# Kernel optimization log

Hardware: AMD Instinct MI355X
Metric: run time of the kernel (lower is better)

The kernel has to match this reference:

```python
import jax, jax.numpy as jnp
import numpy as np

NUM_EMB = 512
EMB_DIM = 64
BETA = 0.25


def _conv(x, w, b, stride, pad):
    # x: NCHW, w: OIHW
    y = jax.lax.conv_general_dilated(
        x, w, window_strides=(stride, stride),
        padding=[(pad, pad), (pad, pad)],
        dimension_numbers=('NCHW', 'OIHW', 'NCHW'))
    return y + b[None, :, None, None]


def _deconv(x, w, b, stride, pad, k):
    # torch ConvTranspose2d weight is [in, out, kh, kw]; flip spatially,
    # swap to OIHW, and run a fractionally-strided (lhs-dilated) conv.
    wt = jnp.flip(w, axis=(2, 3)).transpose(1, 0, 2, 3)
    p = k - 1 - pad
    y = jax.lax.conv_general_dilated(
        x, wt, window_strides=(1, 1),
        padding=[(p, p), (p, p)],
        lhs_dilation=(stride, stride),
        dimension_numbers=('NCHW', 'OIHW', 'NCHW'))
    return y + b[None, :, None, None]


def setup_inputs() -> dict:
    key = jax.random.key(0)
    ks = jax.random.split(key, 16)
    s = 0.05
    inp = {
        'x': jax.random.normal(ks[0], (32, 3, 256, 256), jnp.float32),
        # encoder
        'w1': jax.random.normal(ks[1], (64, 3, 4, 4), jnp.float32) * s,
        'b1': jnp.zeros((64,), jnp.float32),
        'w2': jax.random.normal(ks[2], (128, 64, 4, 4), jnp.float32) * s,
        'b2': jnp.zeros((128,), jnp.float32),
        'w3': jax.random.normal(ks[3], (EMB_DIM, 128, 3, 3), jnp.float32) * s,
        'b3': jnp.zeros((EMB_DIM,), jnp.float32),
        # codebook, uniform(-1/N, 1/N) as in torch init
        'emb': jax.random.uniform(ks[4], (NUM_EMB, EMB_DIM), jnp.float32,
                                  -1.0 / NUM_EMB, 1.0 / NUM_EMB),
        # decoder (ConvTranspose2d weights: [in, out, kh, kw])
        'dw1': jax.random.normal(ks[5], (EMB_DIM, 128, 4, 4), jnp.float32) * s,
        'db1': jnp.zeros((128,), jnp.float32),
        'dw2': jax.random.normal(ks[6], (128, 64, 4, 4), jnp.float32) * s,
        'db2': jnp.zeros((64,), jnp.float32),
        'dw3': jax.random.normal(ks[7], (64, 3, 3, 3), jnp.float32) * s,
        'db3': jnp.zeros((3,), jnp.float32),
    }
    return inp


def _forward(x, w1, b1, w2, b2, w3, b3, emb, dw1, db1, dw2, db2, dw3, db3):
    # encoder
    h = jax.nn.relu(_conv(x, w1, b1, 2, 1))
    h = jax.nn.relu(_conv(h, w2, b2, 2, 1))
    z = jax.nn.relu(_conv(h, w3, b3, 1, 1))      # [B, D, H/4, W/4]
    z = z.transpose(0, 2, 3, 1)                   # NHWC
    # vector quantize
    flat = z.reshape(-1, EMB_DIM)                 # [N, D]
    d = (jnp.sum(flat * flat, axis=1, keepdims=True)
         - 2.0 * flat @ emb.T
         + jnp.sum(emb * emb, axis=1))            # [N, K]
    idx = jnp.argmin(d, axis=1)
    q = emb[idx].reshape(z.shape)
    sg = jax.lax.stop_gradient
    loss = jnp.mean((sg(q) - z) ** 2) + BETA * jnp.mean((q - sg(z)) ** 2)
    q = z + sg(q - z)                             # straight-through
    q = q.transpose(0, 3, 1, 2)                   # NCHW
    # decoder
    h = jax.nn.relu(_deconv(q, dw1, db1, 2, 1, 4))
    h = jax.nn.relu(_deconv(h, dw2, db2, 2, 1, 4))
    x_recon = jax.nn.sigmoid(_deconv(h, dw3, db3, 1, 1, 3))
    return x_recon, loss


def reference(x, w1, b1, w2, b2, w3, b3, emb, dw1, db1, dw2, db2, dw3, db3):
    return _forward(x, w1, b1, w2, b2, w3, b3, emb,
                    dw1, db1, dw2, db2, dw3, db3)
```

## Files before the change

### kernel.cpp

```cpp
#include <hip/hip_runtime.h>
#include <math.h>


typedef __attribute__((ext_vector_type(8))) short bf16x8;
typedef __attribute__((ext_vector_type(4))) float fx4;
typedef unsigned short ushort_t;
#define MFMA16(a, b, c) __builtin_amdgcn_mfma_f32_16x16x32_bf16(a, b, c, 0, 0, 0)

__device__ inline ushort_t f2bf(float f) {
    unsigned u = __float_as_uint(f);
    u += 0x7FFFu + ((u >> 16) & 1u);
    return (ushort_t)(u >> 16);
}
__device__ inline float bf2f(ushort_t h) {
    return __uint_as_float(((unsigned)h) << 16);
}

__device__ __forceinline__ void stage16(const ushort_t* g, ushort_t* l) {
#if __has_builtin(__builtin_amdgcn_global_load_lds)
    __builtin_amdgcn_global_load_lds(
        (const __attribute__((address_space(1))) unsigned int*)g,
        (__attribute__((address_space(3))) unsigned int*)l, 16, 0, 0);
#else
    int lane = threadIdx.x & 63;
    *(int4*)(l + lane * 8) = *(const int4*)g;
#endif
}

__device__ __forceinline__ int swz(int s) { return s ^ ((s >> 3) & 7); }
__device__ __forceinline__ bf16x8 sld(const ushort_t* sm, int gslot) {
    return *(const bf16x8*)(sm + (size_t)swz(gslot) * 8);
}

__device__ __forceinline__ void halo_do(
    ushort_t* __restrict__ buf, int B, int H, int W, int C8, int idx)
{
    int perim = 2 * W + 2 * (H - 2);
    int c8 = idx % C8;
    int t = idx / C8;
    int p = t % perim;
    int b = t / perim;
    int r, col;
    if (p < W) { r = 0; col = p; }
    else if (p < 2 * W) { r = H - 1; col = p - W; }
    else { int pp = p - 2 * W; r = 1 + (pp >> 1); col = (pp & 1) ? (W - 1) : 0; }
    size_t off = ((((size_t)b * H + r) * W + col) * C8 + c8) * 8;
    *(int4*)(buf + off) = (int4){0, 0, 0, 0};
}

__global__ __launch_bounds__(256) void halo3_k(
    ushort_t* __restrict__ xp, ushort_t* __restrict__ h2p, ushort_t* __restrict__ qpad)
{
    int i = blockIdx.x * 256 + threadIdx.x;
    if (i < 132096) halo_do(xp, 32, 130, 130, 8, i);
    else if (i < 265216) halo_do(h2p, 32, 66, 66, 16, i - 132096);
    else if (i < 331776) halo_do(qpad, 32, 66, 66, 8, i - 265216);
}
__global__ __launch_bounds__(256) void halo2_k(
    ushort_t* __restrict__ d1c, ushort_t* __restrict__ d2c)
{
    int i = blockIdx.x * 256 + threadIdx.x;
    if (i < 132096) halo_do(d1c, 16, 130, 130, 16, i);
    else if (i < 263680) halo_do(d2c, 16, 258, 258, 8, i - 132096);
}

__global__ __launch_bounds__(256) void cast_x4(
    const float* __restrict__ x, ushort_t* __restrict__ x4)
{
    if (blockIdx.x < 8192) {
        int i = blockIdx.x * 256 + threadIdx.x;
        int w = i & 255, h = (i >> 8) & 255, b = i >> 16;
        size_t base = ((size_t)b * 3 * 256 + h) * 256 + w;
        float v0 = x[base];
        float v1 = x[base + 65536];
        float v2 = x[base + 131072];
        uint2 o;
        o.x = (unsigned)f2bf(v0) | ((unsigned)f2bf(v1) << 16);
        o.y = (unsigned)f2bf(v2);
        *(uint2*)(x4 + ((size_t)(b * 258 + h + 1) * 258 + (w + 1)) * 4) = o;
    } else {
        int idx = (blockIdx.x - 8192) * 256 + threadIdx.x;
        if (idx >= 32 * 1032) return;
        int b = idx / 1032;
        int s = idx % 1032;
        int side = s / 258, c = s % 258;
        int r, col;
        if (side == 0) { r = 0; col = c; }
        else if (side == 1) { r = 257; col = c; }
        else if (side == 2) { r = c; col = 0; }
        else { r = c; col = 257; }
        *(uint2*)(x4 + ((size_t)(b * 258 + r) * 258 + col) * 4) = (uint2){0, 0};
    }
}

__global__ __launch_bounds__(256) void repack_all(
    const float* __restrict__ w1, const float* __restrict__ w2,
    const float* __restrict__ w3, const float* __restrict__ dw1,
    const float* __restrict__ dw2, const float* __restrict__ dw3,
    const float* __restrict__ emb,
    ushort_t* __restrict__ o1, ushort_t* __restrict__ o2,
    ushort_t* __restrict__ o3, ushort_t* __restrict__ od1,
    ushort_t* __restrict__ od2, ushort_t* __restrict__ od3,
    ushort_t* __restrict__ embb, float* __restrict__ se2,
    float* __restrict__ lac)
{
    int gi = blockIdx.x * 256 + threadIdx.x;
    if (gi < 4096) {
        int i = gi;
        int j = i & 7, lane = (i >> 3) & 63, tc = i >> 9;
        int c = tc & 1, t = tc >> 1;
        int co = t * 16 + (lane & 15);
        int k = c * 32 + (lane >> 4) * 8 + j;
        int kh = k >> 4, kw = (k >> 2) & 3, ci = k & 3;
        o1[i] = (ci < 3) ? f2bf(w1[((co * 3 + ci) * 4 + kh) * 4 + kw]) : (ushort_t)0;
    } else if (gi < 135168) {
        int i = gi - 4096;
        int j = i & 7, lane = (i >> 3) & 63, tc = i >> 9;
        int c = tc & 31, t = tc >> 5;
        int co = t * 16 + (lane & 15);
        int k = c * 32 + (lane >> 4) * 8 + j;
        int tap = k >> 6, ci = k & 63, kh = tap >> 2, kw = tap & 3;
        o2[i] = f2bf(w2[((co * 64 + ci) * 4 + kh) * 4 + kw]);
    } else if (gi < 208896) {
        int i = gi - 135168;
        int j = i & 7, lane = (i >> 3) & 63, tc = i >> 9;
        int c = tc % 36, t = tc / 36;
        int co = t * 16 + (lane & 15);
        int k = c * 32 + (lane >> 4) * 8 + j;
        int tap = k >> 7, ci = k & 127, kh = tap / 3, kw = tap % 3;
        o3[i] = f2bf(w3[((co * 128 + ci) * 3 + kh) * 3 + kw]);
    } else if (gi < 339968) {
        int i = gi - 208896;
        int j = i & 7, lane = (i >> 3) & 63, tc = i >> 9;
        int c = tc & 31, t = tc >> 5;
        int co = t * 16 + (lane & 15);
        int k = c * 32 + (lane >> 4) * 8 + j;
        int tap = k >> 6, ci = k & 63, kh = tap >> 2, kw = tap & 3;
        od1[i] = f2bf(dw1[((ci * 128 + co) * 4 + kh) * 4 + kw]);
    } else if (gi < 471040) {
        int i = gi - 339968;
        int j = i & 7, lane = (i >> 3) & 63, tc = i >> 9;
        int c = tc & 63, t = tc >> 6;
        int co = t * 16 + (lane & 15);
        int k = c * 32 + (lane >> 4) * 8 + j;
        int tap = k >> 7, ci = k & 127, kh = tap >> 2, kw = tap & 3;
        od2[i] = f2bf(dw2[((ci * 64 + co) * 4 + kh) * 4 + kw]);
    } else if (gi < 480256) {
        int i = gi - 471040;
        int j = i & 7, lane = (i >> 3) & 63, c = i >> 9;
        int co = lane & 15;
        int k = c * 32 + (lane >> 4) * 8 + j;
        int tap = k >> 6, ci = k & 63, kh = tap / 3, kw = tap % 3;
        od3[i] = (co < 3) ? f2bf(dw3[((ci * 3 + co) * 3 + kh) * 3 + kw]) : (ushort_t)0;
    } else if (gi < 513024) {
        int i = gi - 480256;
        int j = i & 7, lane = (i >> 3) & 63, c = (i >> 9) & 1, nt = i >> 10;
        int n = nt * 16 + (lane & 15);
        int k = c * 32 + (lane >> 4) * 8 + j;
        embb[i] = f2bf(emb[n * 64 + k]);
    } else if (gi < 513536) {
        int n = gi - 513024;
        const float* e = emb + n * 64;
        float s = 0.f;
        for (int d = 0; d < 64; ++d) s = fmaf(e[d], e[d], s);
        se2[n] = s;
    } else if (gi == 513536) {
        lac[0] = 0.f;
    }
}

__global__ __launch_bounds__(256) void conv1_mfma(
    const ushort_t* __restrict__ x4, const ushort_t* __restrict__ wr,
    const float* __restrict__ bias, ushort_t* __restrict__ xp)
{
    __shared__ ushort_t sm[4608];
    int tid = threadIdx.x;
    int wv = tid >> 6, lane = tid & 63;
    int n16 = lane & 15, quad = lane >> 4;
    int i = blockIdx.x;
    int xcd = i & 7, j = i >> 3;
    int b = j >> 4, oh = xcd * 16 + (j & 15);
    const ushort_t* gsrc = x4 + (size_t)(b * 258 + 2 * oh) * 1032;
    int sl = lane ^ ((lane >> 3) & 7);
    bf16x8 bfr[4][2];
    #pragma unroll
    for (int nt = 0; nt < 4; ++nt)
        #pragma unroll
        for (int c = 0; c < 2; ++c)
            bfr[nt][c] = *(const bf16x8*)(wr + ((size_t)(nt * 2 + c) * 64 + lane) * 8);
    for (int u = wv; u < 9; u += 4)
        stage16(gsrc + u * 512 + sl * 8, sm + u * 512);
    __syncthreads();

    fx4 acc[2][4];
    #pragma unroll
    for (int i2 = 0; i2 < 2; ++i2)
        #pragma unroll
        for (int j2 = 0; j2 < 4; ++j2) acc[i2][j2] = (fx4){0.f, 0.f, 0.f, 0.f};
    #pragma unroll
    for (int c = 0; c < 2; ++c) {
        int kh = 2 * c + (quad >> 1);
        int kwh = quad & 1;
        bf16x8 af[2];
        #pragma unroll
        for (int mt = 0; mt < 2; ++mt) {
            int ow = (wv * 2 + mt) * 16 + n16;
            af[mt] = sld(sm, kh * 129 + ow + kwh);
        }
        #pragma unroll
        for (int mt = 0; mt < 2; ++mt)
            #pragma unroll
            for (int nt = 0; nt < 4; ++nt)
                acc[mt][nt] = MFMA16(af[mt], bfr[nt][c], acc[mt][nt]);
    }
    #pragma unroll
    for (int nt = 0; nt < 4; ++nt) {
        int co = nt * 16 + n16;
        float bs = bias[co];
        #pragma unroll
        for (int mt = 0; mt < 2; ++mt) {
            #pragma unroll
            for (int r = 0; r < 4; ++r) {
                int ow = (wv * 2 + mt) * 16 + quad * 4 + r;
                xp[((size_t)(b * 130 + oh + 1) * 130 + (ow + 1)) * 64 + co] =
                    f2bf(fmaxf(acc[mt][nt][r] + bs, 0.f));
            }
        }
    }
}

__global__ __launch_bounds__(256, 2) void conv2_mfma(
    const ushort_t* __restrict__ xp, const ushort_t* __restrict__ wr,
    const float* __restrict__ bias, ushort_t* __restrict__ h2p)
{
    __shared__ ushort_t sm[33280];
    int tid = threadIdx.x;
    int wv = tid >> 6, lane = tid & 63;
    int n16 = lane & 15, quad = lane >> 4;
    int i = blockIdx.x;
    int xcd = i & 7, j = i >> 3;
    int b = j >> 3, oh = xcd * 8 + (j & 7);
    const ushort_t* gsrc = xp + (size_t)(b * 130 + 2 * oh) * 130 * 64;
    int sl = lane ^ ((lane >> 3) & 7);
    int mg = wv & 1, ng = wv >> 1;

    bf16x8 Bb[8];
    #pragma unroll
    for (int nt = 0; nt < 4; ++nt)
        #pragma unroll
        for (int ks = 0; ks < 2; ++ks)
            Bb[nt * 2 + ks] = *(const bf16x8*)(
                wr + ((size_t)((ng * 4 + nt) * 32 + 0 * 2 + ks) * 64 + lane) * 8);
    for (int u = wv; u < 65; u += 4)
        stage16(gsrc + (size_t)u * 512 + sl * 8, sm + u * 512);
    __syncthreads();

    fx4 acc[2][4];
    #pragma unroll
    for (int i2 = 0; i2 < 2; ++i2)
        #pragma unroll
        for (int j2 = 0; j2 < 4; ++j2) acc[i2][j2] = (fx4){0.f, 0.f, 0.f, 0.f};
    for (int tap = 0; tap < 16; ++tap) {
        if (tap > 0) {
            #pragma unroll
            for (int nt = 0; nt < 4; ++nt)
                #pragma unroll
                for (int ks = 0; ks < 2; ++ks)
                    Bb[nt * 2 + ks] = *(const bf16x8*)(
                        wr + ((size_t)((ng * 4 + nt) * 32 + tap * 2 + ks) * 64 + lane) * 8);
        }
        int kh = tap >> 2, kw = tap & 3;
        #pragma unroll
        for (int ks = 0; ks < 2; ++ks) {
            bf16x8 af[2];
            #pragma unroll
            for (int mt = 0; mt < 2; ++mt) {
                int px = kw + 2 * ((mg * 2 + mt) * 16 + n16);
                af[mt] = sld(sm, (kh * 130 + px) * 8 + ks * 4 + quad);
            }
            #pragma unroll
            for (int mt = 0; mt < 2; ++mt)
                #pragma unroll
                for (int nt = 0; nt < 4; ++nt)
                    acc[mt][nt] = MFMA16(af[mt], Bb[nt * 2 + ks], acc[mt][nt]);
        }
    }
    #pragma unroll
    for (int nt = 0; nt < 4; ++nt) {
        int co = (ng * 4 + nt) * 16 + n16;
        float bs = bias[co];
        #pragma unroll
        for (int mt = 0; mt < 2; ++mt) {
            #pragma unroll
            for (int r = 0; r < 4; ++r) {
                int ow = (mg * 2 + mt) * 16 + quad * 4 + r;
                h2p[((size_t)(b * 66 + oh + 1) * 66 + (ow + 1)) * 128 + co] =
                    f2bf(fmaxf(acc[mt][nt][r] + bs, 0.f));
            }
        }
    }
}

__global__ __launch_bounds__(256, 2) void conv3_mfma(
    const ushort_t* __restrict__ hp, const ushort_t* __restrict__ wr,
    const float* __restrict__ bias, ushort_t* __restrict__ z)
{
    __shared__ ushort_t sm[25600];
    int tid = threadIdx.x;
    int wv = tid >> 6, lane = tid & 63;
    int n16 = lane & 15, quad = lane >> 4;
    int i = blockIdx.x;
    int xcd = i & 7, j = i >> 3;
    int b = j >> 3, oh = xcd * 8 + (j & 7);
    const ushort_t* gsrc = hp + (size_t)(b * 66 + oh) * 66 * 128;
    int sl = lane ^ ((lane >> 3) & 7);
    const ushort_t* wb = wr + ((size_t)wv * 36 * 64 + lane) * 8;
    bf16x8 Bb[36];
    #pragma unroll
    for (int s = 0; s < 36; ++s)
        Bb[s] = *(const bf16x8*)(wb + (size_t)s * 512);
    for (int u = wv; u < 50; u += 4)
        stage16(gsrc + (size_t)u * 512 + sl * 8, sm + u * 512);
    __syncthreads();

    fx4 acc[4];
    #pragma unroll
    for (int i2 = 0; i2 < 4; ++i2) acc[i2] = (fx4){0.f, 0.f, 0.f, 0.f};
    #pragma unroll
    for (int tap = 0; tap < 9; ++tap) {
        int kh = tap / 3, kw = tap % 3;
        #pragma unroll
        for (int ks = 0; ks < 4; ++ks) {
            bf16x8 af[4];
            #pragma unroll
            for (int mt = 0; mt < 4; ++mt) {
                int px = kw + mt * 16 + n16;
                af[mt] = sld(sm, (kh * 66 + px) * 16 + ks * 4 + quad);
            }
            #pragma unroll
            for (int mt = 0; mt < 4; ++mt)
                acc[mt] = MFMA16(af[mt], Bb[tap * 4 + ks], acc[mt]);
        }
    }
    int co = wv * 16 + n16;
    float bs = bias[co];
    #pragma unroll
    for (int mt = 0; mt < 4; ++mt) {
        #pragma unroll
        for (int r = 0; r < 4; ++r) {
            int ow = mt * 16 + quad * 4 + r;
            z[((size_t)(b * 64 + oh) * 64 + ow) * 64 + co] =
                f2bf(fmaxf(acc[mt][r] + bs, 0.f));
        }
    }
}

__global__ __launch_bounds__(256) void vq_mfma(
    const ushort_t* __restrict__ z, const ushort_t* __restrict__ embb,
    const float* __restrict__ emb, const float* __restrict__ se2g,
    ushort_t* __restrict__ qpad, float* __restrict__ loss_acc)
{
    __shared__ ushort_t smz[16384];
    __shared__ float sse2[512];
    __shared__ float red[256];
    int tid = threadIdx.x;
    int wv = tid >> 6, lane = tid & 63;
    int n16 = lane & 15, quad = lane >> 4;
    int blk = blockIdx.x;
    const ushort_t* gsrc = z + (size_t)blk * 16384;
    int sl = lane ^ ((lane >> 3) & 7);
    for (int u = wv; u < 32; u += 4)
        stage16(gsrc + (size_t)u * 512 + sl * 8, smz + u * 512);
    for (int i = tid; i < 512; i += 256) sse2[i] = se2g[i];
    __syncthreads();

    bf16x8 a[4][2];
    #pragma unroll
    for (int mt = 0; mt < 4; ++mt)
        #pragma unroll
        for (int ks = 0; ks < 2; ++ks)
            a[mt][ks] = sld(smz, (wv * 64 + mt * 16 + n16) * 8 + ks * 4 + quad);

    float best[4][4];
    int bid[4][4];
    #pragma unroll
    for (int mt = 0; mt < 4; ++mt)
        #pragma unroll
        for (int r = 0; r < 4; ++r) { best[mt][r] = 1e30f; bid[mt][r] = 0; }

    for (int nt = 0; nt < 32; ++nt) {
        bf16x8 b0 = *(const bf16x8*)(embb + ((size_t)(nt * 2 + 0) * 64 + lane) * 8);
        bf16x8 b1 = *(const bf16x8*)(embb + ((size_t)(nt * 2 + 1) * 64 + lane) * 8);
        float s2 = sse2[nt * 16 + n16];
        int myn = nt * 16 + n16;
        #pragma unroll
        for (int mt = 0; mt < 4; ++mt) {
            fx4 acc = (fx4){0.f, 0.f, 0.f, 0.f};
            acc = MFMA16(a[mt][0], b0, acc);
            acc = MFMA16(a[mt][1], b1, acc);
            #pragma unroll
            for (int r = 0; r < 4; ++r) {
                float sc = fmaf(-2.f, acc[r], s2);
                if (sc < best[mt][r]) { best[mt][r] = sc; bid[mt][r] = myn; }
            }
        }
    }

    float lsum = 0.f;
    #pragma unroll
    for (int mt = 0; mt < 4; ++mt) {
        #pragma unroll
        for (int r = 0; r < 4; ++r) {
            float bs = best[mt][r];
            int bi = bid[mt][r];
            #pragma unroll
            for (int st = 1; st < 16; st <<= 1) {
                float os = __shfl_xor(bs, st, 64);
                int oi = __shfl_xor(bi, st, 64);
                if (os < bs || (os == bs && oi < bi)) { bs = os; bi = oi; }
            }
            int ml = wv * 64 + mt * 16 + quad * 4 + r;
            int pos = blk * 256 + ml;
            int b = pos >> 12, h = (pos >> 6) & 63, w = pos & 63;
            float4 ev = *(const float4*)(emb + (size_t)bi * 64 + n16 * 4);
            int slot = ml * 8 + (n16 >> 1);
            const ushort_t* zp = smz + (size_t)swz(slot) * 8 + (n16 & 1) * 4;
            float d0 = ev.x - bf2f(zp[0]);
            float d1 = ev.y - bf2f(zp[1]);
            float d2 = ev.z - bf2f(zp[2]);
            float d3 = ev.w - bf2f(zp[3]);
            lsum = fmaf(d0, d0, lsum);
            lsum = fmaf(d1, d1, lsum);
            lsum = fmaf(d2, d2, lsum);
            lsum = fmaf(d3, d3, lsum);
            uint2 o;
            o.x = (unsigned)f2bf(ev.x) | ((unsigned)f2bf(ev.y) << 16);
            o.y = (unsigned)f2bf(ev.z) | ((unsigned)f2bf(ev.w) << 16);
            *(uint2*)(qpad + ((size_t)(b * 66 + h + 1) * 66 + (w + 1)) * 64 + n16 * 4) = o;
        }
    }
    red[tid] = lsum;
    __syncthreads();
    for (int s = 128; s > 0; s >>= 1) {
        if (tid < s) red[tid] += red[tid + s];
        __syncthreads();
    }
    if (tid == 0) atomicAdd(loss_acc, red[0]);
}

__global__ void loss_fin_k(const float* __restrict__ acc, float* __restrict__ out)
{
    out[0] = 1.25f * acc[0] / 8388608.0f;
}

__global__ __launch_bounds__(256, 2) void deconv1_mfma(
    const ushort_t* __restrict__ q, const ushort_t* __restrict__ wr,
    const float* __restrict__ bias, ushort_t* __restrict__ d1)
{
    __shared__ ushort_t sm[8704];
    int tid = threadIdx.x;
    int wv = tid >> 6, lane = tid & 63;
    int n16 = lane & 15, quad = lane >> 4;
    int i = blockIdx.x;
    int xcd = i & 7, j = i >> 3;
    int b = j >> 4, oh = xcd * 16 + (j & 15);
    int h0 = (oh + 1) & 1;
    int ihp0 = ((oh + 1 - h0) >> 1) + 1;
    const ushort_t* gsrc = q + (size_t)(b * 66 + ihp0 - 1) * 66 * 64;
    int sl = lane ^ ((lane >> 3) & 7);
    int pw = wv & 1, ng = wv >> 1;
    int q0 = 1 - pw;
    bf16x8 Bb[4][8];
    #pragma unroll
    for (int nt = 0; nt < 4; ++nt) {
        const ushort_t* wb = wr + ((size_t)(ng * 4 + nt) * 32 * 64 + lane) * 8;
        #pragma unroll
        for (int t2 = 0; t2 < 2; ++t2)
            #pragma unroll
            for (int t3 = 0; t3 < 2; ++t3)
                #pragma unroll
                for (int ks = 0; ks < 2; ++ks) {
                    int tap = (h0 + 2 * t2) * 4 + (q0 + 2 * t3);
                    Bb[nt][t2 * 4 + t3 * 2 + ks] =
                        *(const bf16x8*)(wb + (size_t)(tap * 2 + ks) * 512);
                }
    }
    for (int u = wv; u < 17; u += 4)
        stage16(gsrc + (size_t)u * 512 + sl * 8, sm + u * 512);
    __syncthreads();

    fx4 acc[4][4];
    #pragma unroll
    for (int i2 = 0; i2 < 4; ++i2)
        #pragma unroll
        for (int j2 = 0; j2 < 4; ++j2) acc[i2][j2] = (fx4){0.f, 0.f, 0.f, 0.f};
    #pragma unroll
    for (int t2 = 0; t2 < 2; ++t2) {
        int lrow = 1 - t2;
        #pragma unroll
        for (int t3 = 0; t3 < 2; ++t3) {
            int cadd = pw + (t3 == 0 ? 1 : 0);
            #pragma unroll
            for (int ks = 0; ks < 2; ++ks) {
                bf16x8 af[4];
                #pragma unroll
                for (int mt = 0; mt < 4; ++mt) {
                    int px = cadd + mt * 16 + n16;
                    af[mt] = sld(sm, (lrow * 66 + px) * 8 + ks * 4 + quad);
                }
                #pragma unroll
                for (int mt = 0; mt < 4; ++mt)
                    #pragma unroll
                    for (int nt = 0; nt < 4; ++nt)
                        acc[mt][nt] = MFMA16(af[mt], Bb[nt][t2 * 4 + t3 * 2 + ks], acc[mt][nt]);
            }
        }
    }
    #pragma unroll
    for (int nt = 0; nt < 4; ++nt) {
        int co = (ng * 4 + nt) * 16 + n16;
        float bs = bias[co];
        #pragma unroll
        for (int mt = 0; mt < 4; ++mt) {
            #pragma unroll
            for (int r = 0; r < 4; ++r) {
                int ow = 2 * (mt * 16 + quad * 4 + r) + pw;
                d1[((size_t)(b * 130 + oh + 1) * 130 + (ow + 1)) * 128 + co] =
                    f2bf(fmaxf(acc[mt][nt][r] + bs, 0.f));
            }
        }
    }
}

__global__ __launch_bounds__(256, 2) void deconv2_mfma(
    const ushort_t* __restrict__ d1, const ushort_t* __restrict__ wr,
    const float* __restrict__ bias, ushort_t* __restrict__ d2)
{
    __shared__ ushort_t sm[33280];
    int tid = threadIdx.x;
    int wv = tid >> 6, lane = tid & 63;
    int n16 = lane & 15, quad = lane >> 4;
    int i = blockIdx.x;
    int xcd = i & 7, j = i >> 3;
    int b = j >> 5, oh = xcd * 32 + (j & 31);
    int h0 = (oh + 1) & 1;
    int ihp0 = ((oh + 1 - h0) >> 1) + 1;
    const ushort_t* gsrc = d1 + (size_t)(b * 130 + ihp0 - 1) * 130 * 128;
    int sl = lane ^ ((lane >> 3) & 7);
    int pw = wv & 1, mh = wv >> 1;
    int q0 = 1 - pw;

    int taps[4];
    #pragma unroll
    for (int g = 0; g < 4; ++g)
        taps[g] = (h0 + 2 * (g >> 1)) * 4 + (q0 + 2 * (g & 1));

    bf16x8 Bb[16];
    #pragma unroll
    for (int nt = 0; nt < 4; ++nt)
        #pragma unroll
        for (int ks = 0; ks < 4; ++ks)
            Bb[nt * 4 + ks] = *(const bf16x8*)(
                wr + ((size_t)(nt * 64 + taps[0] * 4 + ks) * 64 + lane) * 8);

    for (int u = wv; u < 65; u += 4)
        stage16(gsrc + (size_t)u * 512 + sl * 8, sm + u * 512);
    __syncthreads();

    fx4 acc[4][4];
    #pragma unroll
    for (int i2 = 0; i2 < 4; ++i2)
        #pragma unroll
        for (int j2 = 0; j2 < 4; ++j2) acc[i2][j2] = (fx4){0.f, 0.f, 0.f, 0.f};

    #pragma unroll
    for (int g = 0; g < 4; ++g) {
        if (g > 0) {
            int tapc = taps[g];
            #pragma unroll
            for (int nt = 0; nt < 4; ++nt)
                #pragma unroll
                for (int ks = 0; ks < 4; ++ks)
                    Bb[nt * 4 + ks] = *(const bf16x8*)(
                        wr + ((size_t)(nt * 64 + tapc * 4 + ks) * 64 + lane) * 8);
        }
        int t2 = g >> 1, t3 = g & 1;
        int lrow = 1 - t2;
        int cadd = pw + (t3 == 0 ? 1 : 0);
        #pragma unroll
        for (int ks = 0; ks < 4; ++ks) {
            bf16x8 af[4];
            #pragma unroll
            for (int mt = 0; mt < 4; ++mt) {
                int px = cadd + (mh * 4 + mt) * 16 + n16;
                af[mt] = sld(sm, (lrow * 130 + px) * 16 + ks * 4 + quad);
            }
            #pragma unroll
            for (int mt = 0; mt < 4; ++mt)
                #pragma unroll
                for (int nt = 0; nt < 4; ++nt)
                    acc[mt][nt] = MFMA16(af[mt], Bb[nt * 4 + ks], acc[mt][nt]);
        }
    }

    #pragma unroll
    for (int nt = 0; nt < 4; ++nt) {
        int co = nt * 16 + n16;
        float bs = bias[co];
        #pragma unroll
        for (int mt = 0; mt < 4; ++mt) {
            #pragma unroll
            for (int r = 0; r < 4; ++r) {
                int t = (mh * 4 + mt) * 16 + quad * 4 + r;
                int ow = 2 * t + pw;
                d2[((size_t)(b * 258 + oh + 1) * 258 + (ow + 1)) * 64 + co] =
                    f2bf(fmaxf(acc[mt][nt][r] + bs, 0.f));
            }
        }
    }
}

__global__ __launch_bounds__(256) void deconv3_mfma(
    const ushort_t* __restrict__ d2, const ushort_t* __restrict__ wr,
    const float* __restrict__ bias, float* __restrict__ out)
{
    __shared__ ushort_t sm[26112];
    int tid = threadIdx.x;
    int wv = tid >> 6, lane = tid & 63;
    int n16 = lane & 15, quad = lane >> 4;
    int i = blockIdx.x;
    int xcd = i & 7, j = i >> 3;
    int bh = j >> 5;
    int b = bh >> 1, half = bh & 1;
    int oh = xcd * 32 + (j & 31);
    int sl = lane ^ ((lane >> 3) & 7);
    bf16x8 Bb[18];
    #pragma unroll
    for (int s = 0; s < 18; ++s)
        Bb[s] = *(const bf16x8*)(wr + ((size_t)s * 64 + lane) * 8);
    for (int u = wv; u < 51; u += 4) {
        int c = u / 17, uu = u - c * 17;
        const ushort_t* gsrc = d2 + ((size_t)(b * 258 + oh + c) * 258 + half * 128) * 64;
        stage16(gsrc + (size_t)uu * 512 + sl * 8, sm + c * 8704 + uu * 512);
    }
    __syncthreads();

    fx4 acc[2];
    #pragma unroll
    for (int i2 = 0; i2 < 2; ++i2) acc[i2] = (fx4){0.f, 0.f, 0.f, 0.f};
    #pragma unroll
    for (int tap = 0; tap < 9; ++tap) {
        int kh = tap / 3, kw = tap % 3;
        int c = 2 - kh;
        #pragma unroll
        for (int ks = 0; ks < 2; ++ks) {
            bf16x8 af[2];
            #pragma unroll
            for (int mt = 0; mt < 2; ++mt) {
                int px = (2 - kw) + (wv * 2 + mt) * 16 + n16;
                af[mt] = sld(sm, c * 1088 + px * 8 + ks * 4 + quad);
            }
            #pragma unroll
            for (int mt = 0; mt < 2; ++mt)
                acc[mt] = MFMA16(af[mt], Bb[tap * 2 + ks], acc[mt]);
        }
    }
    int co = n16;
    if (co < 3) {
        float bs = bias[co];
        #pragma unroll
        for (int mt = 0; mt < 2; ++mt) {
            int ow0 = half * 128 + (wv * 2 + mt) * 16 + quad * 4;
            float4 v;
            v.x = 1.f / (1.f + __expf(-(acc[mt][0] + bs)));
            v.y = 1.f / (1.f + __expf(-(acc[mt][1] + bs)));
            v.z = 1.f / (1.f + __expf(-(acc[mt][2] + bs)));
            v.w = 1.f / (1.f + __expf(-(acc[mt][3] + bs)));
            *(float4*)(out + (((size_t)b * 3 + co) * 256 + oh) * 256 + ow0) = v;
        }
    }
}

extern "C" void kernel_launch(void* const* d_in, const int* in_sizes, int n_in,
                              void* d_out, int out_size, void* d_ws, size_t ws_size,
                              hipStream_t stream)
{
    const float* x   = (const float*)d_in[0];
    const float* w1  = (const float*)d_in[1];
    const float* b1  = (const float*)d_in[2];
    const float* w2  = (const float*)d_in[3];
    const float* b2  = (const float*)d_in[4];
    const float* w3  = (const float*)d_in[5];
    const float* b3  = (const float*)d_in[6];
    const float* emb = (const float*)d_in[7];
    const float* dw1 = (const float*)d_in[8];
    const float* db1 = (const float*)d_in[9];
    const float* dw2 = (const float*)d_in[10];
    const float* db2 = (const float*)d_in[11];
    const float* dw3 = (const float*)d_in[12];
    const float* db3 = (const float*)d_in[13];
    float* xout = (float*)d_out;

    ushort_t* shared = (ushort_t*)d_ws;
    ushort_t* xp   = shared;
    ushort_t* h2p  = shared + 34611200;
    ushort_t* d1c  = shared;
    ushort_t* d2c  = shared + 34611200;
    ushort_t* x4   = shared + 94252544;
    ushort_t* zb   = shared + 102772736;
    ushort_t* qpad = zb + 8388608;
    ushort_t* wr1  = qpad + 8921088;
    ushort_t* wr2  = wr1  + 4096;
    ushort_t* wr3  = wr2  + 131072;
    ushort_t* wd1  = wr3  + 73728;
    ushort_t* wd2  = wd1  + 131072;
    ushort_t* wd3  = wd2  + 131072;
    ushort_t* embb = wd3  + 9216;
    float*    se2  = (float*)(embb + 32768);
    float*    lac  = se2 + 512;

    repack_all<<<2007, 256, 0, stream>>>(w1, w2, w3, dw1, dw2, dw3, emb,
                                         wr1, wr2, wr3, wd1, wd2, wd3,
                                         embb, se2, lac);
    cast_x4 <<<8321, 256, 0, stream>>>(x, x4);
    halo3_k <<<1296, 256, 0, stream>>>(xp, h2p, qpad);

    conv1_mfma<<<4096, 256, 0, stream>>>(x4, wr1, b1, xp);
    conv2_mfma<<<2048, 256, 0, stream>>>(xp, wr2, b2, h2p);
    conv3_mfma<<<2048, 256, 0, stream>>>(h2p, wr3, b3, zb);
    vq_mfma   <<<512,  256, 0, stream>>>(zb, embb, emb, se2, qpad, lac);
    loss_fin_k<<<1, 1, 0, stream>>>(lac, xout + 6291456);

    halo2_k<<<1030, 256, 0, stream>>>(d1c, d2c);

    for (int c0 = 0; c0 < 32; c0 += 16) {
        deconv1_mfma<<<2048, 256, 0, stream>>>(qpad + (size_t)c0 * 278784, wd1, db1, d1c);
        deconv2_mfma<<<4096, 256, 0, stream>>>(d1c, wd2, db2, d2c);
        deconv3_mfma<<<8192, 256, 0, stream>>>(d2c, wd3, db3, xout + (size_t)c0 * 196608);
    }
}
```

Measured before the change: 542.1 us.

## Compute two output rows per deconv3 block and add row-dependent LDS swizzle

The final 3x3 deconv kernel now produces two output rows per block. It stages four input rows instead of three, so neighbouring rows share their halo rows, and the grid is halved. The LDS swizzle gains an extra XOR term based on higher address bits in both the staging offset and the read path, applied to every kernel, to spread bank conflicts across rows. The cost is more LDS per block (about 68 KB) with an occupancy hint of 4, and a swizzle that must stay consistent between writer and reader.

```diff
diff --git a/kernel.cpp b/kernel.cpp
--- a/kernel.cpp
+++ b/kernel.cpp
@@ -27,7 +27,12 @@
 #endif
 }
 
-__device__ __forceinline__ int swz(int s) { return s ^ ((s >> 3) & 7); }
+__device__ __forceinline__ int swz(int s) {
+    return s ^ ((s >> 3) & 7) ^ ((s >> 8) & 7);
+}
+__device__ __forceinline__ int ssl(int lane, int u) {
+    return lane ^ ((lane >> 3) & 7) ^ ((u >> 2) & 7);
+}
 __device__ __forceinline__ bf16x8 sld(const ushort_t* sm, int gslot) {
     return *(const bf16x8*)(sm + (size_t)swz(gslot) * 8);
 }
@@ -181,7 +186,6 @@
     int xcd = i & 7, j = i >> 3;
     int b = j >> 4, oh = xcd * 16 + (j & 15);
     const ushort_t* gsrc = x4 + (size_t)(b * 258 + 2 * oh) * 1032;
-    int sl = lane ^ ((lane >> 3) & 7);
     bf16x8 bfr[4][2];
     #pragma unroll
     for (int nt = 0; nt < 4; ++nt)
@@ -189,7 +193,7 @@
         for (int c = 0; c < 2; ++c)
             bfr[nt][c] = *(const bf16x8*)(wr + ((size_t)(nt * 2 + c) * 64 + lane) * 8);
     for (int u = wv; u < 9; u += 4)
-        stage16(gsrc + u * 512 + sl * 8, sm + u * 512);
+        stage16(gsrc + u * 512 + ssl(lane, u) * 8, sm + u * 512);
     __syncthreads();
 
     fx4 acc[2][4];
@@ -241,7 +245,6 @@
     int xcd = i & 7, j = i >> 3;
     int b = j >> 3, oh = xcd * 8 + (j & 7);
     const ushort_t* gsrc = xp + (size_t)(b * 130 + 2 * oh) * 130 * 64;
-    int sl = lane ^ ((lane >> 3) & 7);
     int mg = wv & 1, ng = wv >> 1;
 
     bf16x8 Bb[8];
@@ -252,7 +255,7 @@
             Bb[nt * 2 + ks] = *(const bf16x8*)(
                 wr + ((size_t)((ng * 4 + nt) * 32 + 0 * 2 + ks) * 64 + lane) * 8);
     for (int u = wv; u < 65; u += 4)
-        stage16(gsrc + (size_t)u * 512 + sl * 8, sm + u * 512);
+        stage16(gsrc + (size_t)u * 512 + ssl(lane, u) * 8, sm + u * 512);
     __syncthreads();
 
     fx4 acc[2][4];
@@ -313,14 +316,13 @@
     int xcd = i & 7, j = i >> 3;
     int b = j >> 3, oh = xcd * 8 + (j & 7);
     const ushort_t* gsrc = hp + (size_t)(b * 66 + oh) * 66 * 128;
-    int sl = lane ^ ((lane >> 3) & 7);
     const ushort_t* wb = wr + ((size_t)wv * 36 * 64 + lane) * 8;
     bf16x8 Bb[36];
     #pragma unroll
     for (int s = 0; s < 36; ++s)
         Bb[s] = *(const bf16x8*)(wb + (size_t)s * 512);
     for (int u = wv; u < 50; u += 4)
-        stage16(gsrc + (size_t)u * 512 + sl * 8, sm + u * 512);
+        stage16(gsrc + (size_t)u * 512 + ssl(lane, u) * 8, sm + u * 512);
     __syncthreads();
 
     fx4 acc[4];
@@ -368,9 +370,8 @@
     int n16 = lane & 15, quad = lane >> 4;
     int blk = blockIdx.x;
     const ushort_t* gsrc = z + (size_t)blk * 16384;
-    int sl = lane ^ ((lane >> 3) & 7);
     for (int u = wv; u < 32; u += 4)
-        stage16(gsrc + (size_t)u * 512 + sl * 8, smz + u * 512);
+        stage16(gsrc + (size_t)u * 512 + ssl(lane, u) * 8, smz + u * 512);
     for (int i = tid; i < 512; i += 256) sse2[i] = se2g[i];
     __syncthreads();
 
@@ -467,7 +468,6 @@
     int h0 = (oh + 1) & 1;
     int ihp0 = ((oh + 1 - h0) >> 1) + 1;
     const ushort_t* gsrc = q + (size_t)(b * 66 + ihp0 - 1) * 66 * 64;
-    int sl = lane ^ ((lane >> 3) & 7);
     int pw = wv & 1, ng = wv >> 1;
     int q0 = 1 - pw;
     bf16x8 Bb[4][8];
@@ -486,7 +486,7 @@
                 }
     }
     for (int u = wv; u < 17; u += 4)
-        stage16(gsrc + (size_t)u * 512 + sl * 8, sm + u * 512);
+        stage16(gsrc + (size_t)u * 512 + ssl(lane, u) * 8, sm + u * 512);
     __syncthreads();
 
     fx4 acc[4][4];
@@ -546,7 +546,6 @@
     int h0 = (oh + 1) & 1;
     int ihp0 = ((oh + 1 - h0) >> 1) + 1;
     const ushort_t* gsrc = d1 + (size_t)(b * 130 + ihp0 - 1) * 130 * 128;
-    int sl = lane ^ ((lane >> 3) & 7);
     int pw = wv & 1, mh = wv >> 1;
     int q0 = 1 - pw;
 
@@ -564,7 +563,7 @@
                 wr + ((size_t)(nt * 64 + taps[0] * 4 + ks) * 64 + lane) * 8);
 
     for (int u = wv; u < 65; u += 4)
-        stage16(gsrc + (size_t)u * 512 + sl * 8, sm + u * 512);
+        stage16(gsrc + (size_t)u * 512 + ssl(lane, u) * 8, sm + u * 512);
     __syncthreads();
 
     fx4 acc[4][4];
@@ -620,57 +619,55 @@
     }
 }
 
-__global__ __launch_bounds__(256) void deconv3_mfma(
+__global__ __launch_bounds__(256, 4) void deconv3_mfma(
     const ushort_t* __restrict__ d2, const ushort_t* __restrict__ wr,
     const float* __restrict__ bias, float* __restrict__ out)
 {
-    __shared__ ushort_t sm[26112];
+    __shared__ ushort_t sm[34816];
     int tid = threadIdx.x;
     int wv = tid >> 6, lane = tid & 63;
     int n16 = lane & 15, quad = lane >> 4;
     int i = blockIdx.x;
     int xcd = i & 7, j = i >> 3;
-    int bh = j >> 5;
+    int bh = j >> 4;
     int b = bh >> 1, half = bh & 1;
-    int oh = xcd * 32 + (j & 31);
-    int sl = lane ^ ((lane >> 3) & 7);
+    int oh0 = (xcd * 16 + (j & 15)) * 2;
     bf16x8 Bb[18];
     #pragma unroll
     for (int s = 0; s < 18; ++s)
         Bb[s] = *(const bf16x8*)(wr + ((size_t)s * 64 + lane) * 8);
-    for (int u = wv; u < 51; u += 4) {
+    for (int u = wv; u < 68; u += 4) {
         int c = u / 17, uu = u - c * 17;
-        const ushort_t* gsrc = d2 + ((size_t)(b * 258 + oh + c) * 258 + half * 128) * 64;
-        stage16(gsrc + (size_t)uu * 512 + sl * 8, sm + c * 8704 + uu * 512);
+        const ushort_t* gsrc = d2 + ((size_t)(b * 258 + oh0 + c) * 258 + half * 128) * 64;
+        stage16(gsrc + (size_t)uu * 512 + ssl(lane, u) * 8, sm + u * 512);
     }
     __syncthreads();
 
-    fx4 acc[2];
-    #pragma unroll
-    for (int i2 = 0; i2 < 2; ++i2) acc[i2] = (fx4){0.f, 0.f, 0.f, 0.f};
+    int rr = wv >> 1, mg = wv & 1;
+    fx4 acc[4];
+    #pragma unroll
+    for (int i2 = 0; i2 < 4; ++i2) acc[i2] = (fx4){0.f, 0.f, 0.f, 0.f};
     #pragma unroll
     for (int tap = 0; tap < 9; ++tap) {
         int kh = tap / 3, kw = tap % 3;
-        int c = 2 - kh;
+        int w = rr + 2 - kh;
         #pragma unroll
         for (int ks = 0; ks < 2; ++ks) {
-            bf16x8 af[2];
-            #pragma unroll
-            for (int mt = 0; mt < 2; ++mt) {
-                int px = (2 - kw) + (wv * 2 + mt) * 16 + n16;
-                af[mt] = sld(sm, c * 1088 + px * 8 + ks * 4 + quad);
-            }
-            #pragma unroll
-            for (int mt = 0; mt < 2; ++mt)
-                acc[mt] = MFMA16(af[mt], Bb[tap * 2 + ks], acc[mt]);
+            bf16x8 bfr = Bb[tap * 2 + ks];
+            #pragma unroll
+            for (int mt = 0; mt < 4; ++mt) {
+                int px = (2 - kw) + (mg * 4 + mt) * 16 + n16;
+                acc[mt] = MFMA16(sld(sm, w * 1088 + px * 8 + ks * 4 + quad), bfr, acc[mt]);
+            }
         }
     }
     int co = n16;
     if (co < 3) {
         float bs = bias[co];
-        #pragma unroll
-        for (int mt = 0; mt < 2; ++mt) {
-            int ow0 = half * 128 + (wv * 2 + mt) * 16 + quad * 4;
+        int oh = oh0 + rr;
+        #pragma unroll
+        for (int mt = 0; mt < 4; ++mt) {
+            int ow0 = half * 128 + (mg * 4 + mt) * 16 + quad * 4;
             float4 v;
             v.x = 1.f / (1.f + __expf(-(acc[mt][0] + bs)));
             v.y = 1.f / (1.f + __expf(-(acc[mt][1] + bs)));
@@ -736,6 +733,6 @@
     for (int c0 = 0; c0 < 32; c0 += 16) {
         deconv1_mfma<<<2048, 256, 0, stream>>>(qpad + (size_t)c0 * 278784, wd1, db1, d1c);
         deconv2_mfma<<<4096, 256, 0, stream>>>(d1c, wd2, db2, d2c);
-        deconv3_mfma<<<8192, 256, 0, stream>>>(d2c, wd3, db3, xout + (size_t)c0 * 196608);
-    }
-}
+        deconv3_mfma<<<4096, 256, 0, stream>>>(d2c, wd3, db3, xout + (size_t)c0 * 196608);
+    }
+}
```

After: 549.5 us. About the same (+1.4%).
